# Optimization experiments

Measured on AMD Instinct MI355X. Metric: run time of the kernel, lower is better.

The kernel has to match this reference:

```python
import jax, jax.numpy as jnp
import numpy as np

NEG_INF = jnp.finfo(jnp.float32).min


def _continual_mask(attach_test_after, Q, K, test_num, chunk_size):
    """Boolean allowed-mask [B, 1, Q, K] replicating get_continual_mask +
    the per-batch test-query/train-key override in forward()."""
    k_train = K - test_num * chunk_size
    q_train = Q - test_num * chunk_size
    qi = jnp.arange(Q)[:, None]          # [Q,1]
    kj = jnp.arange(K)[None, :]          # [1,K]
    # base causal mask with diagonal offset K-Q (train queries)
    base = kj <= qi + (K - Q)            # [Q,K]
    # block-diagonal tril for test-query / test-key region
    dq = qi - q_train                    # local test row (negative for train rows, unused there)
    dk = kj - k_train
    block = (kj >= k_train) & (dk <= dq) & ((dk // chunk_size) == (dq // chunk_size))
    # per-batch: test query in chunk n may see train keys <= attach_test_after[b, n]
    chunk_idx = jnp.clip(dq[:, 0], 0, None) // chunk_size          # [Q]
    att = attach_test_after[:, chunk_idx]                          # [B,Q]
    train_key_allowed = kj[None, :, :] <= att[:, :, None]          # [B,Q,K]
    allowed = jnp.where(qi < q_train, base[None],
                        jnp.where(kj[None] < k_train, train_key_allowed, block[None]))
    return allowed[:, None]              # [B,1,Q,K]


def setup_inputs() -> dict:
    key = jax.random.key(0)
    k1, k2, k3, k4 = jax.random.split(key, 4)
    B, L, H, D = 4, 2048, 8, 64
    test_num, train_len = 64, 1536
    return {
        "queries": jax.random.normal(k1, (B, L, H, D), dtype=jnp.float32),
        "keys": jax.random.normal(k2, (B, L, H, D), dtype=jnp.float32),
        "values": jax.random.normal(k3, (B, L, H, D), dtype=jnp.float32),
        "attach_test_after": jax.random.randint(k4, (B, test_num), 0, train_len).astype(jnp.int64),
        "train_len": train_len,
    }


def reference(queries, keys, values, attach_test_after, train_len):
    B, Lq, H, Dqk = queries.shape
    test_num = attach_test_after.shape[1]
    chunk_size = (Lq - train_len) // test_num
    q = jnp.transpose(queries, (0, 2, 1, 3))   # [B,H,Lq,D]
    k = jnp.transpose(keys, (0, 2, 1, 3))      # [B,H,Lk,D]
    v = jnp.transpose(values, (0, 2, 1, 3))    # [B,H,Lk,Dv]
    Lk = k.shape[2]
    # vanilla path: scaled QK^T + continual mask + softmax + AV
    logits = jnp.einsum('bhmd,bhnd->bhmn', q, k) / jnp.sqrt(jnp.float32(Dqk))
    allowed = _continual_mask(attach_test_after, Lq, Lk, test_num, chunk_size)
    logits = jnp.where(allowed, logits, NEG_INF)
    attn = jax.nn.softmax(logits, axis=-1)
    out = jnp.einsum('bhmn,bhnd->bhmd', attn, v)
    return out.transpose(0, 2, 1, 3).reshape(B, Lq, H * v.shape[-1])  # b l (h d)
```

## Files before the change

### kernel.cpp

```cpp
#include <hip/hip_runtime.h>
#include <hip/hip_bf16.h>

typedef __bf16 bf16_t;
typedef __bf16 bf16x8 __attribute__((ext_vector_type(8)));
typedef float  f32x4  __attribute__((ext_vector_type(4)));

#define MFMA16(a, b, c) __builtin_amdgcn_mfma_f32_16x16x32_bf16((a), (b), (c), 0, 0, 0)

constexpr int Bc = 4, Lc = 2048, Hc = 8, Dc = 64;
constexpr int HD = Hc * Dc;
constexpr int TRAINc = 1536;
constexpr int ROWS_BLK = 64;
constexpr int KT = 64;
constexpr int PST = 72;

__global__ void prep_k(const float* __restrict__ K, bf16_t* __restrict__ Kb) {
  size_t g = ((size_t)blockIdx.x * 256 + threadIdx.x) * 8;
  float4 a = *(const float4*)(K + g);
  float4 b = *(const float4*)(K + g + 4);
  bf16x8 v;
  v[0] = (bf16_t)a.x; v[1] = (bf16_t)a.y; v[2] = (bf16_t)a.z; v[3] = (bf16_t)a.w;
  v[4] = (bf16_t)b.x; v[5] = (bf16_t)b.y; v[6] = (bf16_t)b.z; v[7] = (bf16_t)b.w;
  *(bf16x8*)(Kb + g) = v;
}

__global__ void prep_v(const float* __restrict__ V, bf16_t* __restrict__ Vt) {
  __shared__ bf16_t T[64][72];
  const int bid = blockIdx.x;
  const int kt = bid & 31, h = (bid >> 5) & 7, b = bid >> 8;
  const int t = (int)threadIdx.x;
  {
    int kl = t >> 2, dp = (t & 3) << 4;
    const float* s = V + ((size_t)(b * Lc + kt * 64 + kl) * Hc + h) * Dc + dp;
    bf16x8 v0, v1;
    float4 f;
    f = *(const float4*)(s);      v0[0]=(bf16_t)f.x; v0[1]=(bf16_t)f.y; v0[2]=(bf16_t)f.z; v0[3]=(bf16_t)f.w;
    f = *(const float4*)(s + 4);  v0[4]=(bf16_t)f.x; v0[5]=(bf16_t)f.y; v0[6]=(bf16_t)f.z; v0[7]=(bf16_t)f.w;
    f = *(const float4*)(s + 8);  v1[0]=(bf16_t)f.x; v1[1]=(bf16_t)f.y; v1[2]=(bf16_t)f.z; v1[3]=(bf16_t)f.w;
    f = *(const float4*)(s + 12); v1[4]=(bf16_t)f.x; v1[5]=(bf16_t)f.y; v1[6]=(bf16_t)f.z; v1[7]=(bf16_t)f.w;
    *(bf16x8*)&T[kl][dp] = v0;
    *(bf16x8*)&T[kl][dp + 8] = v1;
  }
  __syncthreads();
  {
    int d = t >> 2, kp = (t & 3) << 4;
    bf16x8 o0, o1;
#pragma unroll
    for (int i = 0; i < 8; ++i) { o0[i] = T[kp + i][d]; o1[i] = T[kp + 8 + i][d]; }
    bf16_t* dst = Vt + ((size_t)((b * Hc + h) * Dc + d)) * Lc + kt * 64 + kp;
    *(bf16x8*)dst = o0;
    *(bf16x8*)(dst + 8) = o1;
  }
}

static __device__ __forceinline__ void load16(const bf16_t* g, bf16_t* l) {
  __builtin_amdgcn_global_load_lds(
      (const __attribute__((address_space(1))) unsigned int*)g,
      (__attribute__((address_space(3))) unsigned int*)l, 16, 0, 0);
}

__global__ __launch_bounds__(256, 2)
void continual_attn(const float* __restrict__ Qg, const bf16_t* __restrict__ Kb,
                    const bf16_t* __restrict__ Vt, const int* __restrict__ ATT,
                    float* __restrict__ OUT)
{
  __shared__ __align__(16) bf16_t Klds[2][KT * 64];
  __shared__ __align__(16) bf16_t Vlds[2][Dc * KT];
  __shared__ __align__(16) bf16_t Plds[4][16 * PST];

  const int bid  = blockIdx.x;
  const int qblk = 31 - (bid >> 5);
  const int h    = bid & 7;
  const int b    = (bid >> 3) & 3;
  const int q0   = qblk * ROWS_BLK;

  const int tid  = (int)threadIdx.x;
  const int wave = tid >> 6;
  const int lane = tid & 63;
  const int quad = lane >> 4;
  const int col  = lane & 15;
  const int qw   = q0 + wave * 16;

  const size_t bhQ = (size_t)b * Lc * HD + (size_t)h * Dc;

  const int kr = tid >> 3;
  const bf16_t* ksrcA = Kb + bhQ + (size_t)kr * HD + (((tid & 7) ^ (kr & 7)) << 3);
  const bf16_t* vsrcA = Vt + ((size_t)((b * Hc + h) * Dc + kr)) * Lc + (((tid & 7) ^ (kr & 7)) << 3);
  const bf16_t* vsrcB = vsrcA + (size_t)32 * Lc;

  bf16x8 aq[2];
  {
    const float* qp = Qg + bhQ + (size_t)(qw + col) * HD + quad * 8;
#pragma unroll
    for (int t = 0; t < 2; ++t) {
      float4 lo = *(const float4*)(qp + t * 32);
      float4 hi = *(const float4*)(qp + t * 32 + 4);
      bf16x8 v;
      v[0] = (bf16_t)(lo.x * 0.125f); v[1] = (bf16_t)(lo.y * 0.125f);
      v[2] = (bf16_t)(lo.z * 0.125f); v[3] = (bf16_t)(lo.w * 0.125f);
      v[4] = (bf16_t)(hi.x * 0.125f); v[5] = (bf16_t)(hi.y * 0.125f);
      v[6] = (bf16_t)(hi.z * 0.125f); v[7] = (bf16_t)(hi.w * 0.125f);
      aq[t] = v;
    }
  }

  const bool testblk = (q0 >= TRAINc);
  int kend[4], cstart[4], qir[4];
#pragma unroll
  for (int r = 0; r < 4; ++r) {
    int qi = qw + quad * 4 + r;
    qir[r] = qi;
    if (testblk) {
      kend[r]   = ATT[b * 64 + ((qi - TRAINc) >> 3)] + 1;
      cstart[r] = qi & ~7;
    } else {
      kend[r]   = qi + 1;
      cstart[r] = 0;
    }
  }

  int ntA, ndiag, kfull_end;
  if (testblk) {
    int c0 = (q0 - TRAINc) >> 3;
    int amax = 0, amin = 0x7fffffff;
#pragma unroll
    for (int i = 0; i < 8; ++i) {
      int a = ATT[b * 64 + c0 + i];
      amax = (a > amax) ? a : amax;
      amin = (a < amin) ? a : amin;
    }
    ntA = (amax >> 6) + 1;
    ndiag = 1;
    kfull_end = amin + 1;
  } else {
    ntA = qblk + 1;
    ndiag = 0;
    kfull_end = q0 + 1;
  }
  const int ntot = ntA + ndiag;

  float lsumL[4] = {0.f, 0.f, 0.f, 0.f};
  f32x4 o[4] = {{0,0,0,0},{0,0,0,0},{0,0,0,0},{0,0,0,0}};

  const int cA = ((quad ^ (col & 7)) << 3);

  {
    bf16_t* kd = Klds[0];
    bf16_t* vd = Vlds[0];
    load16(ksrcA, kd + wave * 512);
    load16(ksrcA + (size_t)32 * HD, kd + 2048 + wave * 512);
    load16(vsrcA, vd + wave * 512);
    load16(vsrcB, vd + 2048 + wave * 512);
  }

  for (int ti = 0; ti < ntot; ++ti) {
    const int buf = ti & 1;
    __syncthreads();

    if (ti + 1 < ntot) {
      const int kn = (ti + 1 < ntA) ? (ti + 1) * KT : q0 + (ti + 1 - ntA) * KT;
      bf16_t* kd = Klds[1 - buf];
      bf16_t* vd = Vlds[1 - buf];
      load16(ksrcA + (size_t)kn * HD, kd + wave * 512);
      load16(ksrcA + (size_t)(kn + 32) * HD, kd + 2048 + wave * 512);
      load16(vsrcA + kn, vd + wave * 512);
      load16(vsrcB + kn, vd + 2048 + wave * 512);
    }

    const bf16_t* kb = Klds[buf];
    const bf16_t* vbuf = Vlds[buf];
    const int k0 = (ti < ntA) ? ti * KT : q0 + (ti - ntA) * KT;

    f32x4 sf[4] = {{0,0,0,0},{0,0,0,0},{0,0,0,0},{0,0,0,0}};
#pragma unroll
    for (int kg = 0; kg < 4; ++kg) {
      const bf16_t* krow = kb + (kg * 16 + col) * 64;
      bf16x8 k0f = *(const bf16x8*)(krow + cA);
      bf16x8 k1f = *(const bf16x8*)(krow + (cA ^ 32));
      sf[kg] = MFMA16(aq[0], k0f, sf[kg]);
      sf[kg] = MFMA16(aq[1], k1f, sf[kg]);
    }

    const int mode = (ti >= ntA) ? 2 : ((k0 + KT <= kfull_end) ? 0 : 1);
    if (mode == 1) {
#pragma unroll
      for (int kg = 0; kg < 4; ++kg) {
        const int kgv = k0 + kg * 16 + col;
#pragma unroll
        for (int r = 0; r < 4; ++r)
          if (kgv >= kend[r]) sf[kg][r] = -1e30f;
      }
    } else if (mode == 2) {
#pragma unroll
      for (int kg = 0; kg < 4; ++kg) {
        const int kgv = k0 + kg * 16 + col;
#pragma unroll
        for (int r = 0; r < 4; ++r)
          if (kgv < cstart[r] || kgv > qir[r]) sf[kg][r] = -1e30f;
      }
    }

    bf16_t* pw = Plds[wave];
#pragma unroll
    for (int kg = 0; kg < 4; ++kg) {
#pragma unroll
      for (int r = 0; r < 4; ++r) {
        float p = __expf(sf[kg][r]);
        lsumL[r] += p;
        pw[(quad * 4 + r) * PST + kg * 16 + col] = (bf16_t)p;
      }
    }
    bf16x8 pa0 = *(const bf16x8*)&pw[col * PST + quad * 8];
    bf16x8 pa1 = *(const bf16x8*)&pw[col * PST + 32 + quad * 8];

#pragma unroll
    for (int t = 0; t < 4; ++t) {
      const bf16_t* vrow = vbuf + (t * 16 + col) * 64;
      bf16x8 v0 = *(const bf16x8*)(vrow + cA);
      bf16x8 v1 = *(const bf16x8*)(vrow + (cA ^ 32));
      o[t] = MFMA16(pa0, v0, o[t]);
      o[t] = MFMA16(pa1, v1, o[t]);
    }
  }

#pragma unroll
  for (int r = 0; r < 4; ++r) {
    float rs = lsumL[r];
    rs += __shfl_xor(rs, 1);
    rs += __shfl_xor(rs, 2);
    rs += __shfl_xor(rs, 4);
    rs += __shfl_xor(rs, 8);
    float inv = 1.f / rs;
    int qi = qw + quad * 4 + r;
    float* op = OUT + ((size_t)b * Lc + qi) * HD + (size_t)h * Dc + col;
    op[0]  = o[0][r] * inv;
    op[16] = o[1][r] * inv;
    op[32] = o[2][r] * inv;
    op[48] = o[3][r] * inv;
  }
}

extern "C" void kernel_launch(void* const* d_in, const int* in_sizes, int n_in,
                              void* d_out, int out_size, void* d_ws, size_t ws_size,
                              hipStream_t stream) {
  const float* Q   = (const float*)d_in[0];
  const float* K   = (const float*)d_in[1];
  const float* V   = (const float*)d_in[2];
  const int*   ATT = (const int*)d_in[3];
  float* OUT = (float*)d_out;
  (void)in_sizes; (void)n_in; (void)out_size; (void)ws_size;

  const size_t NE = (size_t)Bc * Lc * Hc * Dc;
  bf16_t* Kb = (bf16_t*)d_ws;
  bf16_t* Vt = Kb + NE;

  prep_k<<<dim3((unsigned)(NE / 8 / 256)), dim3(256), 0, stream>>>(K, Kb);
  prep_v<<<dim3(Bc * Hc * (Lc / 64)), dim3(256), 0, stream>>>(V, Vt);
  continual_attn<<<dim3(Bc * Hc * (Lc / ROWS_BLK)), dim3(256), 0, stream>>>(Q, Kb, Vt, ATT, OUT);
}
```

Measured before the change: 132.4 us.

## Fuse K/V prep kernels, swizzle LDS tiles, raise occupancy, add MFMA priority

Merges the K conversion and V transpose kernels into one launch, so one launch and the gap between the two kernels go away. The padded LDS layouts for the V transpose and the P tile are replaced with XOR-swizzled unpadded layouts, which cuts LDS use and is meant to avoid bank conflicts. Launch bounds go from 2 to 4 blocks per SM, which can force register pressure or spills. s_setprio is placed around the MFMA loops to favour matrix issue between waves.

After: 131.8 us. About the same (-0.4%).

```diff
diff --git a/kernel.cpp b/kernel.cpp
--- a/kernel.cpp
+++ b/kernel.cpp
@@ -12,23 +12,27 @@
 constexpr int TRAINc = 1536;
 constexpr int ROWS_BLK = 64;
 constexpr int KT = 64;
-constexpr int PST = 72;
-
-__global__ void prep_k(const float* __restrict__ K, bf16_t* __restrict__ Kb) {
-  size_t g = ((size_t)blockIdx.x * 256 + threadIdx.x) * 8;
-  float4 a = *(const float4*)(K + g);
-  float4 b = *(const float4*)(K + g + 4);
-  bf16x8 v;
-  v[0] = (bf16_t)a.x; v[1] = (bf16_t)a.y; v[2] = (bf16_t)a.z; v[3] = (bf16_t)a.w;
-  v[4] = (bf16_t)b.x; v[5] = (bf16_t)b.y; v[6] = (bf16_t)b.z; v[7] = (bf16_t)b.w;
-  *(bf16x8*)(Kb + g) = v;
-}
-
-__global__ void prep_v(const float* __restrict__ V, bf16_t* __restrict__ Vt) {
-  __shared__ bf16_t T[64][72];
-  const int bid = blockIdx.x;
+
+constexpr int PREPK_BLOCKS = (int)((size_t)Bc * Lc * Hc * Dc / 8 / 256);
+
+__global__ void prep_fused(const float* __restrict__ K, bf16_t* __restrict__ Kb,
+                           const float* __restrict__ V, bf16_t* __restrict__ Vt) {
+  __shared__ bf16_t T[64][64];
+  const int t = (int)threadIdx.x;
+
+  if ((int)blockIdx.x < PREPK_BLOCKS) {
+    size_t g = ((size_t)blockIdx.x * 256 + t) * 8;
+    float4 a = *(const float4*)(K + g);
+    float4 b = *(const float4*)(K + g + 4);
+    bf16x8 v;
+    v[0] = (bf16_t)a.x; v[1] = (bf16_t)a.y; v[2] = (bf16_t)a.z; v[3] = (bf16_t)a.w;
+    v[4] = (bf16_t)b.x; v[5] = (bf16_t)b.y; v[6] = (bf16_t)b.z; v[7] = (bf16_t)b.w;
+    *(bf16x8*)(Kb + g) = v;
+    return;
+  }
+
+  const int bid = (int)blockIdx.x - PREPK_BLOCKS;
   const int kt = bid & 31, h = (bid >> 5) & 7, b = bid >> 8;
-  const int t = (int)threadIdx.x;
   {
     int kl = t >> 2, dp = (t & 3) << 4;
     const float* s = V + ((size_t)(b * Lc + kt * 64 + kl) * Hc + h) * Dc + dp;
@@ -38,15 +42,22 @@
     f = *(const float4*)(s + 4);  v0[4]=(bf16_t)f.x; v0[5]=(bf16_t)f.y; v0[6]=(bf16_t)f.z; v0[7]=(bf16_t)f.w;
     f = *(const float4*)(s + 8);  v1[0]=(bf16_t)f.x; v1[1]=(bf16_t)f.y; v1[2]=(bf16_t)f.z; v1[3]=(bf16_t)f.w;
     f = *(const float4*)(s + 12); v1[4]=(bf16_t)f.x; v1[5]=(bf16_t)f.y; v1[6]=(bf16_t)f.z; v1[7]=(bf16_t)f.w;
-    *(bf16x8*)&T[kl][dp] = v0;
-    *(bf16x8*)&T[kl][dp + 8] = v1;
+    const int x = kl >> 3;
+    const int c0 = dp >> 3;
+    *(bf16x8*)&T[kl][(c0 ^ x) << 3]       = v0;
+    *(bf16x8*)&T[kl][((c0 + 1) ^ x) << 3] = v1;
   }
   __syncthreads();
   {
     int d = t >> 2, kp = (t & 3) << 4;
+    const int xa = kp >> 3;
+    const int xb = xa + 1;
+    const int lo = d & 7, hi = d >> 3;
+    const int x0 = ((hi ^ xa) << 3) + lo;
+    const int x1 = ((hi ^ xb) << 3) + lo;
     bf16x8 o0, o1;
 #pragma unroll
-    for (int i = 0; i < 8; ++i) { o0[i] = T[kp + i][d]; o1[i] = T[kp + 8 + i][d]; }
+    for (int i = 0; i < 8; ++i) { o0[i] = T[kp + i][x0]; o1[i] = T[kp + 8 + i][x1]; }
     bf16_t* dst = Vt + ((size_t)((b * Hc + h) * Dc + d)) * Lc + kt * 64 + kp;
     *(bf16x8*)dst = o0;
     *(bf16x8*)(dst + 8) = o1;
@@ -59,14 +70,14 @@
       (__attribute__((address_space(3))) unsigned int*)l, 16, 0, 0);
 }
 
-__global__ __launch_bounds__(256, 2)
+__global__ __launch_bounds__(256, 4)
 void continual_attn(const float* __restrict__ Qg, const bf16_t* __restrict__ Kb,
                     const bf16_t* __restrict__ Vt, const int* __restrict__ ATT,
                     float* __restrict__ OUT)
 {
   __shared__ __align__(16) bf16_t Klds[2][KT * 64];
   __shared__ __align__(16) bf16_t Vlds[2][Dc * KT];
-  __shared__ __align__(16) bf16_t Plds[4][16 * PST];
+  __shared__ __align__(16) bf16_t Plds[4][16 * 64];
 
   const int bid  = blockIdx.x;
   const int qblk = 31 - (bid >> 5);
@@ -143,6 +154,8 @@
   f32x4 o[4] = {{0,0,0,0},{0,0,0,0},{0,0,0,0},{0,0,0,0}};
 
   const int cA = ((quad ^ (col & 7)) << 3);
+  const int c7 = col & 7;
+  const int c8 = col >> 3;
 
   {
     bf16_t* kd = Klds[0];
@@ -172,6 +185,7 @@
     const int k0 = (ti < ntA) ? ti * KT : q0 + (ti - ntA) * KT;
 
     f32x4 sf[4] = {{0,0,0,0},{0,0,0,0},{0,0,0,0},{0,0,0,0}};
+    __builtin_amdgcn_s_setprio(1);
 #pragma unroll
     for (int kg = 0; kg < 4; ++kg) {
       const bf16_t* krow = kb + (kg * 16 + col) * 64;
@@ -180,6 +194,7 @@
       sf[kg] = MFMA16(aq[0], k0f, sf[kg]);
       sf[kg] = MFMA16(aq[1], k1f, sf[kg]);
     }
+    __builtin_amdgcn_s_setprio(0);
 
     const int mode = (ti >= ntA) ? 2 : ((k0 + KT <= kfull_end) ? 0 : 1);
     if (mode == 1) {
@@ -207,12 +222,14 @@
       for (int r = 0; r < 4; ++r) {
         float p = __expf(sf[kg][r]);
         lsumL[r] += p;
-        pw[(quad * 4 + r) * PST + kg * 16 + col] = (bf16_t)p;
+        const int row = quad * 4 + r;
+        pw[row * 64 + (((2 * kg + c8) ^ (row & 7)) << 3) + c7] = (bf16_t)p;
       }
     }
-    bf16x8 pa0 = *(const bf16x8*)&pw[col * PST + quad * 8];
-    bf16x8 pa1 = *(const bf16x8*)&pw[col * PST + 32 + quad * 8];
-
+    bf16x8 pa0 = *(const bf16x8*)&pw[col * 64 + ((quad ^ c7) << 3)];
+    bf16x8 pa1 = *(const bf16x8*)&pw[col * 64 + (((4 + quad) ^ c7) << 3)];
+
+    __builtin_amdgcn_s_setprio(1);
 #pragma unroll
     for (int t = 0; t < 4; ++t) {
       const bf16_t* vrow = vbuf + (t * 16 + col) * 64;
@@ -221,6 +238,7 @@
       o[t] = MFMA16(pa0, v0, o[t]);
       o[t] = MFMA16(pa1, v1, o[t]);
     }
+    __builtin_amdgcn_s_setprio(0);
   }
 
 #pragma unroll
@@ -254,7 +272,6 @@
   bf16_t* Kb = (bf16_t*)d_ws;
   bf16_t* Vt = Kb + NE;
 
-  prep_k<<<dim3((unsigned)(NE / 8 / 256)), dim3(256), 0, stream>>>(K, Kb);
-  prep_v<<<dim3(Bc * Hc * (Lc / 64)), dim3(256), 0, stream>>>(V, Vt);
+  prep_fused<<<dim3((unsigned)(PREPK_BLOCKS + Bc * Hc * (Lc / 64))), dim3(256), 0, stream>>>(K, Kb, V, Vt);
   continual_attn<<<dim3(Bc * Hc * (Lc / ROWS_BLK)), dim3(256), 0, stream>>>(Q, Kb, Vt, ATT, OUT);
 }
```
